# Kernel tuning notes

Measured on AMD Instinct MI355X. Metric: run time of the kernel, lower is better.

Reference implementation:

```python
import jax, jax.numpy as jnp
import numpy as np

D_MODEL = 1024
N_HEAD = 16
D_FF = 4096
B, S = 2, 2048


def _layernorm(x, g, b, eps=1e-5):
    mu = jnp.mean(x, axis=-1, keepdims=True)
    var = jnp.var(x, axis=-1, keepdims=True)
    return (x - mu) * jax.lax.rsqrt(var + eps) * g + b


def setup_inputs() -> dict:
    key = jax.random.key(0)
    ks = jax.random.split(key, 12)
    s = 0.02
    return {
        "x": jax.random.normal(ks[0], (B, S, D_MODEL), dtype=jnp.float32),
        "src_mask": jnp.zeros((B, 1, 1, S), dtype=jnp.float32),
        "w_q": jax.random.normal(ks[1], (D_MODEL, D_MODEL), dtype=jnp.float32) * s,
        "b_q": jnp.zeros((D_MODEL,), dtype=jnp.float32),
        "w_k": jax.random.normal(ks[2], (D_MODEL, D_MODEL), dtype=jnp.float32) * s,
        "b_k": jnp.zeros((D_MODEL,), dtype=jnp.float32),
        "w_v": jax.random.normal(ks[3], (D_MODEL, D_MODEL), dtype=jnp.float32) * s,
        "b_v": jnp.zeros((D_MODEL,), dtype=jnp.float32),
        "w_o": jax.random.normal(ks[4], (D_MODEL, D_MODEL), dtype=jnp.float32) * s,
        "b_o": jnp.zeros((D_MODEL,), dtype=jnp.float32),
        "w_ff1": jax.random.normal(ks[5], (D_MODEL, D_FF), dtype=jnp.float32) * s,
        "b_ff1": jnp.zeros((D_FF,), dtype=jnp.float32),
        "w_ff2": jax.random.normal(ks[6], (D_FF, D_MODEL), dtype=jnp.float32) * s,
        "b_ff2": jnp.zeros((D_MODEL,), dtype=jnp.float32),
        "ln1_g": jnp.ones((D_MODEL,), dtype=jnp.float32),
        "ln1_b": jnp.zeros((D_MODEL,), dtype=jnp.float32),
        "ln2_g": jnp.ones((D_MODEL,), dtype=jnp.float32),
        "ln2_b": jnp.zeros((D_MODEL,), dtype=jnp.float32),
    }


def reference(x, src_mask, w_q, b_q, w_k, b_k, w_v, b_v, w_o, b_o,
              w_ff1, b_ff1, w_ff2, b_ff2, ln1_g, ln1_b, ln2_g, ln2_b):
    b, s, d = x.shape
    dh = d // N_HEAD

    def split(t):  # [b,s,d] -> [b,h,s,dh]
        return t.reshape(b, s, N_HEAD, dh).transpose(0, 2, 1, 3)

    q = split(x @ w_q + b_q)
    k = split(x @ w_k + b_k)
    v = split(x @ w_v + b_v)

    # naive full-score attention, as in the source module
    score = jnp.einsum('bhqd,bhkd->bhqk', q, k) / jnp.sqrt(jnp.float32(dh))
    score = score + src_mask
    attn = jax.nn.softmax(score, axis=-1)
    out = jnp.einsum('bhqk,bhkd->bhqd', attn, v)
    out = out.transpose(0, 2, 1, 3).reshape(b, s, d)
    out = out @ w_o + b_o

    x = _layernorm(x + out, ln1_g, ln1_b)

    ff = jax.nn.relu(x @ w_ff1 + b_ff1) @ w_ff2 + b_ff2
    x = _layernorm(x + ff, ln2_g, ln2_b)
    return x
```

## Files before the change

### kernel.cpp

```cpp
#include <hip/hip_runtime.h>
#include <cstdint>
#include <cstddef>

#define BATCH 2
#define SEQ 2048
#define DMODEL 1024
#define NHEAD 16
#define DFF 4096
#define MTOT (BATCH * SEQ)

typedef __bf16 bf16x8 __attribute__((ext_vector_type(8)));
typedef __bf16 bf16x4 __attribute__((ext_vector_type(4)));
typedef short s16x4 __attribute__((ext_vector_type(4)));
typedef float f32x4 __attribute__((ext_vector_type(4)));

__device__ __forceinline__ void gload_lds16(const void* g, void* l) {
  __builtin_amdgcn_global_load_lds(
      (__attribute__((address_space(1))) void*)(uintptr_t)g,
      (__attribute__((address_space(3))) void*)(uint32_t)(uintptr_t)l,
      16, 0, 0);
}

__global__ __launch_bounds__(256) void k_transpose_to_bf16(
    const float* __restrict__ w, __bf16* __restrict__ wt, int K, int N) {
  __shared__ float t[32][33];
  const int n0 = blockIdx.x * 32, k0 = blockIdx.y * 32;
  const int tx = threadIdx.x & 31, ty = threadIdx.x >> 5;
#pragma unroll
  for (int i = ty; i < 32; i += 8) t[i][tx] = w[(size_t)(k0 + i) * N + n0 + tx];
  __syncthreads();
#pragma unroll
  for (int i = ty; i < 32; i += 8)
    wt[(size_t)(n0 + i) * K + k0 + tx] = (__bf16)t[tx][i];
}

__global__ __launch_bounds__(256) void k_cvt_bf16(
    const float* __restrict__ in, __bf16* __restrict__ out, int n) {
  const int i = (blockIdx.x * 256 + threadIdx.x) * 4;
  if (i >= n) return;
  const float4 v = *(const float4*)(in + i);
  bf16x4 r;
  r[0] = (__bf16)v.x; r[1] = (__bf16)v.y; r[2] = (__bf16)v.z; r[3] = (__bf16)v.w;
  *(bf16x4*)(out + i) = r;
}

__global__ void k_concat3(const float* __restrict__ a, const float* __restrict__ b,
                          const float* __restrict__ c, float* __restrict__ o) {
  const int i = blockIdx.x * 256 + threadIdx.x;
  if (i >= 3072) return;
  o[i] = (i < 1024) ? a[i] : (i < 2048) ? b[i - 1024] : c[i - 2048];
}

__global__ __launch_bounds__(256) void k_transpose_v(
    const __bf16* __restrict__ qkvb, __bf16* __restrict__ vT) {
  __shared__ __bf16 t[32][33];
  const int s0 = blockIdx.x * 32, c0 = blockIdx.y * 32, b = blockIdx.z;
  const int tx = threadIdx.x & 31, ty = threadIdx.x >> 5;
#pragma unroll
  for (int i = ty; i < 32; i += 8)
    t[i][tx] = qkvb[(size_t)(b * SEQ + s0 + i) * 3072 + 2048 + c0 + tx];
  __syncthreads();
#pragma unroll
  for (int i = ty; i < 32; i += 8)
    vT[((size_t)b * 1024 + c0 + i) * SEQ + s0 + tx] = t[tx][i];
}

template <int MF, bool RELU, typename OutT>
__global__ __launch_bounds__(256) void k_gemm(
    const __bf16* __restrict__ A, const __bf16* __restrict__ BT,
    const float* __restrict__ bias, OutT* __restrict__ C, int M, int N, int K) {
  __shared__ __bf16 sA[MF * 32 * 64];
  __shared__ __bf16 sB[128 * 64];
  const int tid = threadIdx.x, lane = tid & 63, wv = tid >> 6;
  const int wm = wv >> 1, wn = wv & 1;
  const int lrow = lane & 15, hi = lane >> 4;
  const int nwg = gridDim.x * gridDim.y;
  const int flat = blockIdx.y * gridDim.x + blockIdx.x;
  const int cpx = nwg >> 3;
  const int swzb = (flat & 7) * cpx + (flat >> 3);
  const int m0 = (swzb / gridDim.x) * (MF * 32);
  const int n0 = (swzb % gridDim.x) * 128;
  const int srow = lane >> 3;
  const int scolE = ((lane & 7) ^ srow) * 8;
  const int swz = (lrow & 7) << 4;

  f32x4 acc[MF][4];
#pragma unroll
  for (int r = 0; r < MF; ++r)
#pragma unroll
    for (int c = 0; c < 4; ++c) acc[r][c] = f32x4{0.f, 0.f, 0.f, 0.f};

  for (int k0 = 0; k0 < K; k0 += 64) {
    __syncthreads();
#pragma unroll
    for (int rb = wv; rb < MF * 4; rb += 4) {
      const int row = rb * 8 + srow;
      gload_lds16(A + (size_t)(m0 + row) * K + k0 + scolE, &sA[rb * 512]);
    }
#pragma unroll
    for (int rb = wv; rb < 16; rb += 4) {
      const int row = rb * 8 + srow;
      gload_lds16(BT + (size_t)(n0 + row) * K + k0 + scolE, &sB[rb * 512]);
    }
    __syncthreads();
#pragma unroll
    for (int kc = 0; kc < 2; ++kc) {
      bf16x8 af[MF], bfr[4];
#pragma unroll
      for (int r = 0; r < MF; ++r) {
        const int row = wm * (MF * 16) + r * 16 + lrow;
        af[r] = *(const bf16x8*)((const char*)sA + row * 128 + ((kc * 64 + hi * 16) ^ swz));
      }
#pragma unroll
      for (int c = 0; c < 4; ++c) {
        const int row = wn * 64 + c * 16 + lrow;
        bfr[c] = *(const bf16x8*)((const char*)sB + row * 128 + ((kc * 64 + hi * 16) ^ swz));
      }
#pragma unroll
      for (int r = 0; r < MF; ++r)
#pragma unroll
        for (int c = 0; c < 4; ++c)
          acc[r][c] = __builtin_amdgcn_mfma_f32_16x16x32_bf16(af[r], bfr[c],
                                                              acc[r][c], 0, 0, 0);
    }
  }

#pragma unroll
  for (int r = 0; r < MF; ++r) {
    const int row = m0 + wm * (MF * 16) + r * 16 + hi * 4;
#pragma unroll
    for (int c = 0; c < 4; ++c) {
      const int col = n0 + wn * 64 + c * 16 + lrow;
      const float bb = bias[col];
#pragma unroll
      for (int j = 0; j < 4; ++j) {
        float v = acc[r][c][j] + bb;
        if (RELU) v = fmaxf(v, 0.f);
        C[(size_t)(row + j) * N + col] = (OutT)v;
      }
    }
  }
}

__global__ __launch_bounds__(256) void k_attn(
    const __bf16* __restrict__ qkv, const __bf16* __restrict__ vT,
    const float* __restrict__ mask, __bf16* __restrict__ out) {
  const int qb = blockIdx.x, h = blockIdx.y, b = blockIdx.z;
  const int tid = threadIdx.x, lane = tid & 63, wv = tid >> 6;
  const int lrow = lane & 15, hi = lane >> 4;

  __shared__ __bf16 sK[2][64 * 64];
  __shared__ __bf16 sV[2][64 * 64];

  const size_t base = (size_t)b * SEQ * 3072;
  const __bf16* Qb = qkv + base + h * 64;
  const __bf16* Kb = qkv + base + 1024 + h * 64;
  const __bf16* vTb = vT + ((size_t)b * 1024 + h * 64) * SEQ;
  const float* maskb = mask + (size_t)b * SEQ;

  const int q0 = qb * 64 + wv * 16;
  const bf16x8 qf0 = *(const bf16x8*)&Qb[(size_t)(q0 + lrow) * 3072 + hi * 8];
  const bf16x8 qf1 = *(const bf16x8*)&Qb[(size_t)(q0 + lrow) * 3072 + 32 + hi * 8];

  float m_r = -3e38f, l_r = 0.f;
  f32x4 o[4];
#pragma unroll
  for (int d = 0; d < 4; ++d) o[d] = f32x4{0.f, 0.f, 0.f, 0.f};

  const int srow = lane >> 3;
  const int scolE = ((lane & 7) ^ srow) * 8;
  const int swz = (lrow & 7) << 4;

  auto stage = [&](int t) {
    const int k0s = t * 64;
    __bf16* dK = sK[t & 1];
    __bf16* dV = sV[t & 1];
#pragma unroll
    for (int r = 0; r < 2; ++r) {
      const int rb = r * 4 + wv;
      const int row = rb * 8 + srow;
      gload_lds16(Kb + (size_t)(k0s + row) * 3072 + scolE, &dK[rb * 512]);
      gload_lds16(vTb + (size_t)row * SEQ + k0s + scolE, &dV[rb * 512]);
    }
  };

  stage(0);
  const int NT = SEQ / 64;
  for (int t = 0; t < NT; ++t) {
    __syncthreads();
    if (t + 1 < NT) stage(t + 1);
    const __bf16* cK = sK[t & 1];
    const __bf16* cV = sV[t & 1];
    const int k0 = t * 64;

    f32x4 st[4];
#pragma unroll
    for (int t4 = 0; t4 < 4; ++t4) {
      const char* rp = (const char*)cK + (t4 * 16 + lrow) * 128;
      const bf16x8 ka = *(const bf16x8*)(rp + ((hi * 16) ^ swz));
      const bf16x8 kb = *(const bf16x8*)(rp + ((64 + hi * 16) ^ swz));
      f32x4 a = f32x4{0.f, 0.f, 0.f, 0.f};
      a = __builtin_amdgcn_mfma_f32_16x16x32_bf16(ka, qf0, a, 0, 0, 0);
      a = __builtin_amdgcn_mfma_f32_16x16x32_bf16(kb, qf1, a, 0, 0, 0);
      st[t4] = a;
    }

    float pm = -3e38f;
#pragma unroll
    for (int t4 = 0; t4 < 4; ++t4) {
      const f32x4 mk = *(const f32x4*)&maskb[k0 + t4 * 16 + hi * 4];
#pragma unroll
      for (int j = 0; j < 4; ++j) {
        st[t4][j] = st[t4][j] * 0.125f + mk[j];
        pm = fmaxf(pm, st[t4][j]);
      }
    }
    pm = fmaxf(pm, __shfl_xor(pm, 16));
    pm = fmaxf(pm, __shfl_xor(pm, 32));

    const float mn = fmaxf(m_r, pm);
    const float so = __expf(m_r - mn);
    m_r = mn;
    float rs = 0.f;
#pragma unroll
    for (int t4 = 0; t4 < 4; ++t4)
#pragma unroll
      for (int j = 0; j < 4; ++j) {
        st[t4][j] = __expf(st[t4][j] - mn);
        rs += st[t4][j];
      }
    rs += __shfl_xor(rs, 16);
    rs += __shfl_xor(rs, 32);
    l_r = l_r * so + rs;

    float so_o[4];
#pragma unroll
    for (int jj = 0; jj < 4; ++jj) so_o[jj] = __shfl(so, hi * 4 + jj);
#pragma unroll
    for (int d = 0; d < 4; ++d)
#pragma unroll
      for (int jj = 0; jj < 4; ++jj) o[d][jj] *= so_o[jj];

    s16x4 pa[4];
#pragma unroll
    for (int t4 = 0; t4 < 4; ++t4)
#pragma unroll
      for (int j = 0; j < 4; ++j) {
        const __bf16 pb = (__bf16)st[t4][j];
        pa[t4][j] = __builtin_bit_cast(short, pb);
      }

#pragma unroll
    for (int d = 0; d < 4; ++d) {
      const char* rp = (const char*)cV + (d * 16 + lrow) * 128;
#pragma unroll
      for (int t4 = 0; t4 < 4; ++t4) {
        const s16x4 vb = *(const s16x4*)(rp + ((t4 * 32 + hi * 8) ^ swz));
        o[d] = __builtin_amdgcn_mfma_f32_16x16x16bf16_1k(pa[t4], vb, o[d], 0, 0, 0);
      }
    }
  }

  __syncthreads();
  float linv[4];
#pragma unroll
  for (int jj = 0; jj < 4; ++jj) linv[jj] = 1.0f / __shfl(l_r, hi * 4 + jj);
#pragma unroll
  for (int d = 0; d < 4; ++d)
#pragma unroll
    for (int jj = 0; jj < 4; ++jj)
      out[((size_t)b * SEQ + q0 + hi * 4 + jj) * DMODEL + h * 64 + d * 16 + lrow] =
          (__bf16)(o[d][jj] * linv[jj]);
}

__global__ __launch_bounds__(256) void k_add_ln(
    const float* __restrict__ x, const float* __restrict__ y,
    const float* __restrict__ g, const float* __restrict__ be,
    float* __restrict__ of, __bf16* __restrict__ ob) {
  const int row = blockIdx.x, tid = threadIdx.x;
  const float4 a = ((const float4*)(x + (size_t)row * 1024))[tid];
  const float4 b = ((const float4*)(y + (size_t)row * 1024))[tid];
  const float v0 = a.x + b.x, v1 = a.y + b.y, v2 = a.z + b.z, v3 = a.w + b.w;
  float s = v0 + v1 + v2 + v3;
  float s2 = v0 * v0 + v1 * v1 + v2 * v2 + v3 * v3;
#pragma unroll
  for (int off = 32; off > 0; off >>= 1) {
    s += __shfl_xor(s, off);
    s2 += __shfl_xor(s2, off);
  }
  __shared__ float red[2][4];
  const int wv = tid >> 6, lane = tid & 63;
  if (lane == 0) { red[0][wv] = s; red[1][wv] = s2; }
  __syncthreads();
  s = red[0][0] + red[0][1] + red[0][2] + red[0][3];
  s2 = red[1][0] + red[1][1] + red[1][2] + red[1][3];
  const float mean = s * (1.0f / 1024.0f);
  const float var = s2 * (1.0f / 1024.0f) - mean * mean;
  const float rstd = rsqrtf(var + 1e-5f);
  const float4 gg = ((const float4*)g)[tid];
  const float4 bt = ((const float4*)be)[tid];
  float4 r;
  r.x = (v0 - mean) * rstd * gg.x + bt.x;
  r.y = (v1 - mean) * rstd * gg.y + bt.y;
  r.z = (v2 - mean) * rstd * gg.z + bt.z;
  r.w = (v3 - mean) * rstd * gg.w + bt.w;
  ((float4*)(of + (size_t)row * 1024))[tid] = r;
  if (ob) {
    bf16x4 rb;
    rb[0] = (__bf16)r.x; rb[1] = (__bf16)r.y; rb[2] = (__bf16)r.z; rb[3] = (__bf16)r.w;
    *(bf16x4*)(ob + (size_t)row * 1024 + tid * 4) = rb;
  }
}

extern "C" void kernel_launch(void* const* d_in, const int* in_sizes, int n_in,
                              void* d_out, int out_size, void* d_ws, size_t ws_size,
                              hipStream_t stream) {
  const float* x = (const float*)d_in[0];
  const float* src_mask = (const float*)d_in[1];
  const float* w_q = (const float*)d_in[2];
  const float* b_q = (const float*)d_in[3];
  const float* w_k = (const float*)d_in[4];
  const float* b_k = (const float*)d_in[5];
  const float* w_v = (const float*)d_in[6];
  const float* b_v = (const float*)d_in[7];
  const float* w_o = (const float*)d_in[8];
  const float* b_o = (const float*)d_in[9];
  const float* w_ff1 = (const float*)d_in[10];
  const float* b_ff1 = (const float*)d_in[11];
  const float* w_ff2 = (const float*)d_in[12];
  const float* b_ff2 = (const float*)d_in[13];
  const float* ln1_g = (const float*)d_in[14];
  const float* ln1_b = (const float*)d_in[15];
  const float* ln2_g = (const float*)d_in[16];
  const float* ln2_b = (const float*)d_in[17];

  char* ws = (char*)d_ws;
  constexpr size_t O_WQKVT = 0;
  constexpr size_t O_WOT = O_WQKVT + 3072ull * 1024 * 2;
  constexpr size_t O_WFF1T = O_WOT + 1024ull * 1024 * 2;
  constexpr size_t O_WFF2T = O_WFF1T + 4096ull * 1024 * 2;
  constexpr size_t O_BQKV = O_WFF2T + 4096ull * 1024 * 2;
  constexpr size_t O_XBF = O_BQKV + 3072ull * 4;
  constexpr size_t O_QKV = O_XBF + 4096ull * 1024 * 2;
  constexpr size_t O_ATTN = O_QKV + 4096ull * 3072 * 2;
  constexpr size_t O_PROJ = O_ATTN + 4096ull * 1024 * 2;
  constexpr size_t O_H1F = O_PROJ + 4096ull * 1024 * 4;
  constexpr size_t O_H1B = O_H1F + 4096ull * 1024 * 4;
  constexpr size_t O_VT = O_PROJ;
  constexpr size_t O_FF = O_QKV;
  constexpr size_t O_FF2 = O_PROJ;

  __bf16* wqkvT = (__bf16*)(ws + O_WQKVT);
  __bf16* woT = (__bf16*)(ws + O_WOT);
  __bf16* wff1T = (__bf16*)(ws + O_WFF1T);
  __bf16* wff2T = (__bf16*)(ws + O_WFF2T);
  float* bqkv = (float*)(ws + O_BQKV);
  __bf16* xbf = (__bf16*)(ws + O_XBF);
  __bf16* qkvb = (__bf16*)(ws + O_QKV);
  __bf16* attnb = (__bf16*)(ws + O_ATTN);
  float* proj = (float*)(ws + O_PROJ);
  float* h1f = (float*)(ws + O_H1F);
  __bf16* h1b = (__bf16*)(ws + O_H1B);
  __bf16* vT = (__bf16*)(ws + O_VT);
  __bf16* ffb = (__bf16*)(ws + O_FF);
  float* ff2 = (float*)(ws + O_FF2);

  k_transpose_to_bf16<<<dim3(32, 32), 256, 0, stream>>>(w_q, wqkvT, 1024, 1024);
  k_transpose_to_bf16<<<dim3(32, 32), 256, 0, stream>>>(w_k, wqkvT + 1024 * 1024, 1024, 1024);
  k_transpose_to_bf16<<<dim3(32, 32), 256, 0, stream>>>(w_v, wqkvT + 2 * 1024 * 1024, 1024, 1024);
  k_transpose_to_bf16<<<dim3(32, 32), 256, 0, stream>>>(w_o, woT, 1024, 1024);
  k_transpose_to_bf16<<<dim3(128, 32), 256, 0, stream>>>(w_ff1, wff1T, 1024, 4096);
  k_transpose_to_bf16<<<dim3(32, 128), 256, 0, stream>>>(w_ff2, wff2T, 4096, 1024);
  k_concat3<<<12, 256, 0, stream>>>(b_q, b_k, b_v, bqkv);
  k_cvt_bf16<<<4096, 256, 0, stream>>>(x, xbf, MTOT * DMODEL);

  k_gemm<4, false, __bf16><<<dim3(24, 32), 256, 0, stream>>>(xbf, wqkvT, bqkv, qkvb,
                                                             MTOT, 3072, 1024);
  k_transpose_v<<<dim3(64, 32, 2), 256, 0, stream>>>(qkvb, vT);
  k_attn<<<dim3(SEQ / 64, NHEAD, BATCH), 256, 0, stream>>>(qkvb, vT, src_mask, attnb);
  k_gemm<2, false, float><<<dim3(8, 64), 256, 0, stream>>>(attnb, woT, b_o, proj,
                                                           MTOT, 1024, 1024);
  k_add_ln<<<4096, 256, 0, stream>>>(x, proj, ln1_g, ln1_b, h1f, h1b);
  k_gemm<4, true, __bf16><<<dim3(32, 32), 256, 0, stream>>>(h1b, wff1T, b_ff1, ffb,
                                                            MTOT, DFF, 1024);
  k_gemm<2, false, float><<<dim3(8, 64), 256, 0, stream>>>(ffb, wff2T, b_ff2, ff2,
                                                           MTOT, 1024, DFF);
  k_add_ln<<<4096, 256, 0, stream>>>(h1f, ff2, ln2_g, ln2_b, (float*)d_out, nullptr);
}
```

Measured before the change: 288.7 us.

## Add 256x256 tile GEMM with deep LDS pipeline for QKV and FF1

```diff
diff --git a/kernel.cpp b/kernel.cpp
--- a/kernel.cpp
+++ b/kernel.cpp
@@ -13,6 +13,12 @@
 typedef __bf16 bf16x4 __attribute__((ext_vector_type(4)));
 typedef short s16x4 __attribute__((ext_vector_type(4)));
 typedef float f32x4 __attribute__((ext_vector_type(4)));
+
+#define S_BARRIER() __builtin_amdgcn_s_barrier()
+#define SCHED_FENCE() __builtin_amdgcn_sched_barrier(0)
+#define VMCNT8() asm volatile("s_waitcnt vmcnt(8)" ::: "memory")
+#define VMCNT4() asm volatile("s_waitcnt vmcnt(4)" ::: "memory")
+#define VMCNT0() asm volatile("s_waitcnt vmcnt(0)" ::: "memory")
 
 __device__ __forceinline__ void gload_lds16(const void* g, void* l) {
   __builtin_amdgcn_global_load_lds(
@@ -63,6 +69,93 @@
 #pragma unroll
   for (int i = ty; i < 32; i += 8)
     vT[((size_t)b * 1024 + c0 + i) * SEQ + s0 + tx] = t[tx][i];
+}
+
+template <bool RELU, typename OutT>
+__global__ __launch_bounds__(512) void k_gemm256(
+    const __bf16* __restrict__ A, const __bf16* __restrict__ BT,
+    const float* __restrict__ bias, OutT* __restrict__ C,
+    int M, int N, int K) {
+  __shared__ __align__(16) __bf16 sA[4 * 8192];
+  __shared__ __align__(16) __bf16 sB[4 * 8192];
+  const int tid = threadIdx.x, lane = tid & 63, wv = tid >> 6;
+  const int wm = wv >> 2, wn = wv & 3;
+  const int lrow = lane & 15, hi = lane >> 4;
+  const int nwg = gridDim.x * gridDim.y;
+  const int flat = blockIdx.y * gridDim.x + blockIdx.x;
+  const int cpx = nwg >> 3;
+  const int swzb = (flat & 7) * cpx + (flat >> 3);
+  const int m0 = (swzb / gridDim.x) * 256;
+  const int n0 = (swzb % gridDim.x) * 256;
+  const int NT = K >> 6;
+
+  const int lsub = lane >> 2;
+  const int gg = (lane & 3) ^ ((lane >> 3) & 3);
+  const int gr = hi ^ ((lrow >> 1) & 3);
+
+  f32x4 acc[8][4];
+#pragma unroll
+  for (int r = 0; r < 8; ++r)
+#pragma unroll
+    for (int c = 0; c < 4; ++c) acc[r][c] = f32x4{0.f, 0.f, 0.f, 0.f};
+
+  auto stage = [&](int p) {
+    const int tile = p >> 1;
+    const int slot = (((tile & 1) * 2) + (p & 1)) * 8192;
+    const int kcol = tile * 64 + (p & 1) * 32 + gg * 8;
+#pragma unroll
+    for (int i = 0; i < 2; ++i) {
+      const int c = wv * 2 + i;
+      gload_lds16(A + (size_t)(m0 + c * 16 + lsub) * K + kcol, &sA[slot + c * 512]);
+      gload_lds16(BT + (size_t)(n0 + c * 16 + lsub) * K + kcol, &sB[slot + c * 512]);
+    }
+  };
+
+  auto compute = [&](int p) {
+    const int slot = ((((p >> 1) & 1) * 2) + (p & 1)) * 8192;
+    bf16x8 af[8], bfv[4];
+#pragma unroll
+    for (int r = 0; r < 8; ++r)
+      af[r] = *(const bf16x8*)&sA[slot + (wm * 128 + r * 16 + lrow) * 32 + gr * 8];
+#pragma unroll
+    for (int c = 0; c < 4; ++c)
+      bfv[c] = *(const bf16x8*)&sB[slot + (wn * 64 + c * 16 + lrow) * 32 + gr * 8];
+    __builtin_amdgcn_s_setprio(1);
+#pragma unroll
+    for (int r = 0; r < 8; ++r)
+#pragma unroll
+      for (int c = 0; c < 4; ++c)
+        acc[r][c] = __builtin_amdgcn_mfma_f32_16x16x32_bf16(af[r], bfv[c],
+                                                            acc[r][c], 0, 0, 0);
+    __builtin_amdgcn_s_setprio(0);
+  };
+
+  stage(0); stage(1); stage(2);
+  int p = 0;
+  for (; p < 2 * NT - 3; ++p) {
+    VMCNT8(); S_BARRIER(); SCHED_FENCE();
+    stage(p + 3);
+    compute(p);
+  }
+  VMCNT8(); S_BARRIER(); SCHED_FENCE(); compute(p); ++p;
+  VMCNT4(); S_BARRIER(); SCHED_FENCE(); compute(p); ++p;
+  VMCNT0(); S_BARRIER(); SCHED_FENCE(); compute(p);
+
+#pragma unroll
+  for (int r = 0; r < 8; ++r) {
+    const int row = m0 + wm * 128 + r * 16 + hi * 4;
+#pragma unroll
+    for (int c = 0; c < 4; ++c) {
+      const int col = n0 + wn * 64 + c * 16 + lrow;
+      const float bb = bias[col];
+#pragma unroll
+      for (int j = 0; j < 4; ++j) {
+        float v = acc[r][c][j] + bb;
+        if (RELU) v = fmaxf(v, 0.f);
+        C[(size_t)(row + j) * N + col] = (OutT)v;
+      }
+    }
+  }
 }
 
 template <int MF, bool RELU, typename OutT>
@@ -374,14 +467,14 @@
   k_concat3<<<12, 256, 0, stream>>>(b_q, b_k, b_v, bqkv);
   k_cvt_bf16<<<4096, 256, 0, stream>>>(x, xbf, MTOT * DMODEL);
 
-  k_gemm<4, false, __bf16><<<dim3(24, 32), 256, 0, stream>>>(xbf, wqkvT, bqkv, qkvb,
+  k_gemm256<false, __bf16><<<dim3(12, 16), 512, 0, stream>>>(xbf, wqkvT, bqkv, qkvb,
                                                              MTOT, 3072, 1024);
   k_transpose_v<<<dim3(64, 32, 2), 256, 0, stream>>>(qkvb, vT);
   k_attn<<<dim3(SEQ / 64, NHEAD, BATCH), 256, 0, stream>>>(qkvb, vT, src_mask, attnb);
   k_gemm<2, false, float><<<dim3(8, 64), 256, 0, stream>>>(attnb, woT, b_o, proj,
                                                            MTOT, 1024, 1024);
   k_add_ln<<<4096, 256, 0, stream>>>(x, proj, ln1_g, ln1_b, h1f, h1b);
-  k_gemm<4, true, __bf16><<<dim3(32, 32), 256, 0, stream>>>(h1b, wff1T, b_ff1, ffb,
+  k_gemm256<true, __bf16><<<dim3(16, 16), 512, 0, stream>>>(h1b, wff1T, b_ff1, ffb,
                                                             MTOT, DFF, 1024);
   k_gemm<2, false, float><<<dim3(8, 64), 256, 0, stream>>>(ffb, wff2T, b_ff2, ff2,
                                                            MTOT, 1024, DFF);
```

After: 277.1 us. -4.0%, faster.
